# Performance work log

Hardware: AMD Instinct MI355X
Metric: run time of the kernel (lower is better)

The kernel has to match this reference:

```python
import jax, jax.numpy as jnp
import numpy as np

ENERGY_PERCENT = 0.8


def setup_inputs() -> dict:
    key = jax.random.key(0)
    B, T, C = 32, 4096, 128
    x = jax.random.normal(key, (B, T, C), dtype=jnp.float32)
    return {"x": x}


def reference(x):
    # x: [B, T, C]; FFT along time axis.
    T = x.shape[1]
    xf = jnp.fft.rfft(x, axis=1)                      # [B, F, C] complex
    energies = jnp.abs(xf) ** 2                       # [B, F, C]

    # Sort energies descending along freq axis (per batch, per channel).
    sorted_indices = jnp.argsort(-energies, axis=1)   # [B, F, C] int
    sorted_energies = jnp.take_along_axis(energies, sorted_indices, axis=1)

    total_energy = jnp.sum(energies, axis=1, keepdims=True)        # [B, 1, C]
    cumulative = jnp.cumsum(sorted_energies, axis=1)               # [B, F, C]

    # Smallest k such that cumulative energy exceeds energy_percent of total.
    exceeded = cumulative > total_energy * ENERGY_PERCENT          # [B, F, C] bool
    k = jnp.argmax(exceeded, axis=1) + 1                           # [B, C]

    # rank[b, f, c] = position of frequency f in the descending energy order;
    # this is the inverse permutation of sorted_indices (argsort of a permutation).
    rank = jnp.argsort(sorted_indices, axis=1)                     # [B, F, C]

    is_low_freq = rank < k[:, None, :]                             # [B, F, C]

    # Zero out the high-energy ("low-frequency") components -> residual x_var.
    mask = jnp.where(is_low_freq, 0.0, 1.0).astype(x.dtype)        # [B, F, C]
    x_var = jnp.fft.irfft(xf * mask, n=T, axis=1)                  # [B, T, C]
    x_inv = x - x_var
    return (x_var, x_inv)
```

## Files before the change

kernel.cpp:

```cpp
#include <hip/hip_runtime.h>


#define TLEN 4096
#define N2   2048
#define CCH  128
#define BB   32
#define NSER (BB * CCH)
#define HALF 16777216
#define PI_F 3.14159265358979323846f
#define NT   64
#define TS   64
#define SLAB (CCH * TS)

#define LP(i) ((i) + ((i) >> 5))

__device__ __forceinline__ void cmul(float& r, float& i, float br, float bi) {
  float tr = r * br - i * bi;
  i = r * bi + i * br;
  r = tr;
}

__device__ __forceinline__ void dft4(float vr[4], float vi[4], float s) {
  float t0r = vr[0] + vr[2], t0i = vi[0] + vi[2];
  float t1r = vr[0] - vr[2], t1i = vi[0] - vi[2];
  float t2r = vr[1] + vr[3], t2i = vi[1] + vi[3];
  float d3r = vr[1] - vr[3], d3i = vi[1] - vi[3];
  float t3r = -s * d3i, t3i = s * d3r;
  vr[0] = t0r + t2r; vi[0] = t0i + t2i;
  vr[1] = t1r + t3r; vi[1] = t1i + t3i;
  vr[2] = t0r - t2r; vi[2] = t0i - t2i;
  vr[3] = t1r - t3r; vi[3] = t1i - t3i;
}

__device__ __forceinline__ void dft8(float vr[8], float vi[8], float s) {
  float er[4]  = {vr[0], vr[2], vr[4], vr[6]};
  float ei[4]  = {vi[0], vi[2], vi[4], vi[6]};
  float odr[4] = {vr[1], vr[3], vr[5], vr[7]};
  float odi[4] = {vi[1], vi[3], vi[5], vi[7]};
  dft4(er, ei, s);
  dft4(odr, odi, s);
  const float c = 0.70710678118654752440f;
  float wr[4] = {1.0f, c, 0.0f, -c};
  float wi[4] = {0.0f, s * c, s, s * c};
  #pragma unroll
  for (int k = 0; k < 4; ++k) {
    float tr = wr[k] * odr[k] - wi[k] * odi[k];
    float ti = wr[k] * odi[k] + wi[k] * odr[k];
    vr[k]     = er[k] + tr; vi[k]     = ei[k] + ti;
    vr[k + 4] = er[k] - tr; vi[k + 4] = ei[k] - ti;
  }
}

__device__ __forceinline__ void stage8_first(float* zr, float* zi, int tid, float s) {
  float vr[8], vi[8];
  #pragma unroll
  for (int r = 0; r < 8; ++r) {
    int idx = LP(tid + (r << 8));
    vr[r] = zr[idx]; vi[r] = zi[idx];
  }
  dft8(vr, vi, s);
  __syncthreads();
  #pragma unroll
  for (int r = 0; r < 8; ++r) {
    int idx = LP((tid << 3) + r);
    zr[idx] = vr[r]; zi[idx] = vi[r];
  }
  __syncthreads();
}

template <int NS>
__device__ __forceinline__ void stage8_tw(float* zr, float* zi, int tid, float s) {
  int j = tid;
  int p = j & (NS - 1);
  float vr[8], vi[8];
  #pragma unroll
  for (int r = 0; r < 8; ++r) {
    int idx = LP(j + (r << 8));
    vr[r] = zr[idx]; vi[r] = zi[idx];
  }
  float ang = s * 6.28318530717958647692f * (float)p / (float)(NS * 8);
  float s1, c1; __sincosf(ang, &s1, &c1);
  float c2 = c1 * c1 - s1 * s1, s2 = 2.0f * c1 * s1;
  float c3 = c2 * c1 - s2 * s1, s3 = c2 * s1 + s2 * c1;
  float c4 = c2 * c2 - s2 * s2, s4 = 2.0f * c2 * s2;
  float c5 = c4 * c1 - s4 * s1, s5 = c4 * s1 + s4 * c1;
  float c6 = c4 * c2 - s4 * s2, s6 = c4 * s2 + s4 * c2;
  float c7 = c4 * c3 - s4 * s3, s7 = c4 * s3 + s4 * c3;
  cmul(vr[1], vi[1], c1, s1);
  cmul(vr[2], vi[2], c2, s2);
  cmul(vr[3], vi[3], c3, s3);
  cmul(vr[4], vi[4], c4, s4);
  cmul(vr[5], vi[5], c5, s5);
  cmul(vr[6], vi[6], c6, s6);
  cmul(vr[7], vi[7], c7, s7);
  dft8(vr, vi, s);
  __syncthreads();
  int idxD = ((j - p) << 3) + p;
  #pragma unroll
  for (int r = 0; r < 8; ++r) {
    int idx = LP(idxD + r * NS);
    zr[idx] = vr[r]; zi[idx] = vi[r];
  }
  __syncthreads();
}

__device__ __forceinline__ void stage4_last(float* zr, float* zi, int tid, float s) {
  #pragma unroll
  for (int half = 0; half < 2; ++half) {
    int j = tid + (half << 8);
    float ang = s * PI_F * (float)j * (1.0f / 1024.0f);
    float s1, c1; __sincosf(ang, &s1, &c1);
    float c2 = c1 * c1 - s1 * s1, s2 = 2.0f * c1 * s1;
    float c3 = c2 * c1 - s2 * s1, s3 = c2 * s1 + s2 * c1;
    float vr[4], vi[4];
    #pragma unroll
    for (int r = 0; r < 4; ++r) {
      int idx = LP(j + (r << 9));
      vr[r] = zr[idx]; vi[r] = zi[idx];
    }
    cmul(vr[1], vi[1], c1, s1);
    cmul(vr[2], vi[2], c2, s2);
    cmul(vr[3], vi[3], c3, s3);
    dft4(vr, vi, s);
    #pragma unroll
    for (int r = 0; r < 4; ++r) {
      int idx = LP(j + (r << 9));
      zr[idx] = vr[r]; zi[idx] = vi[r];
    }
  }
  __syncthreads();
}

__device__ __forceinline__ void fft2048(float* zr, float* zi, int tid, float s) {
  stage8_first(zr, zi, tid, s);
  stage8_tw<8>(zr, zi, tid, s);
  stage8_tw<64>(zr, zi, tid, s);
  stage4_last(zr, zi, tid, s);
}

__device__ __forceinline__ float block_sum(float v, float* red, int tid, int bank) {
  #pragma unroll
  for (int o = 32; o > 0; o >>= 1) v += __shfl_down(v, o, 64);
  if ((tid & 63) == 0) red[(bank << 2) + (tid >> 6)] = v;
  __syncthreads();
  int b4 = bank << 2;
  return red[b4] + red[b4 + 1] + red[b4 + 2] + red[b4 + 3];
}

__global__ __launch_bounds__(256, 8) void fourier_filter_series(const float* __restrict__ x,
                                                                float* __restrict__ buf) {
  __shared__ float zr[2113], zi[2113];
  __shared__ float red[8];
  int tid = threadIdx.x;

  int bid = blockIdx.x;
  int r = bid & 7;
  int m = bid >> 3;
  int b = m >> 4;
  int u = m & 15;
  int c = (((r + b) & 7) << 4) | u;

  const float* xp = x + ((size_t)b * TLEN) * CCH + c;
  #pragma unroll
  for (int jb = 0; jb < 2; ++jb) {
    float re[4], im[4];
    #pragma unroll
    for (int j = 0; j < 4; ++j) {
      int k = tid + (((jb << 2) + j) << 8);
      int off = k << 8;
      re[j] = xp[off];
      im[j] = xp[off + CCH];
    }
    #pragma unroll
    for (int j = 0; j < 4; ++j) {
      int k = tid + (((jb << 2) + j) << 8);
      zr[LP(k)] = re[j];
      zi[LP(k)] = im[j];
    }
  }
  __syncthreads();

  fft2048(zr, zi, tid, -1.0f);

  float eb[9];
  eb[8] = 0.0f;
  const float RC  = 0.92387953251128675613f;
  const float RSn = -0.38268343236508977173f;
  float ws, wc;
  __sincosf(-PI_F * (float)tid * (1.0f / 2048.0f), &ws, &wc);
  #pragma unroll
  for (int jj = 0; jj < 4; ++jj) {
    int k = tid + (jj << 8);
    int mkz = (N2 - k) & (N2 - 1);
    int ik = LP(k), im = LP(N2 - k);
    float akr = zr[ik],      aki = zi[ik];
    float bkr = zr[LP(mkz)], bki = zi[LP(mkz)];
    float Er  = 0.5f * (akr + bkr);
    float Ei  = 0.5f * (aki - bki);
    float Or_ = 0.5f * (aki + bki);
    float Oi  = 0.5f * (bkr - akr);
    float tr = wc * Or_ - ws * Oi;
    float ti = wc * Oi + ws * Or_;
    float x0r = Er + tr, x0i = Ei + ti;
    float x1r = Er - tr, x1i = ti - Ei;
    zr[ik] = x0r; zi[ik] = x0i;
    zr[im] = x1r; zi[im] = x1i;
    eb[2 * jj]     = x0r * x0r + x0i * x0i;
    eb[2 * jj + 1] = x1r * x1r + x1i * x1i;
    float nwc = wc * RC - ws * RSn;
    ws = wc * RSn + ws * RC; wc = nwc;
  }
  if (tid == 0) {
    int i4 = LP(1024);
    float re = zr[i4], im_ = zi[i4];
    zi[i4] = -im_;
    eb[8] = re * re + im_ * im_;
  }

  float tloc = 0.0f;
  #pragma unroll
  for (int s = 0; s < 9; ++s) tloc += eb[s];
  float total = block_sum(tloc, red, tid, 0);
  float thresh = 0.8f * total;

  unsigned lo = 0u, hi = 0x7F7FFFFFu;
  for (int it = 0; it < 31; ++it) {
    unsigned mid = (lo + hi + 1u) >> 1;
    float tau = __uint_as_float(mid);
    float loc = 0.0f;
    #pragma unroll
    for (int s = 0; s < 9; ++s) loc += (eb[s] >= tau) ? eb[s] : 0.0f;
    float ssum = block_sum(loc, red, tid, (it + 1) & 1);
    if (ssum > thresh) lo = mid; else hi = mid - 1;
  }
  float tau = __uint_as_float(lo);

  const float RSp = 0.38268343236508977173f;
  __sincosf(PI_F * (float)tid * (1.0f / 2048.0f), &ws, &wc);
  #pragma unroll
  for (int jj = 0; jj < 4; ++jj) {
    int k = tid + (jj << 8);
    int ik = LP(k), im = LP(N2 - k);
    float xkr = zr[ik], xki = zi[ik];
    float xmr = zr[im], xmi = zi[im];
    float ekk = xkr * xkr + xki * xki;
    float emm = xmr * xmr + xmi * xmi;
    if (ekk >= tau) { xkr = 0.0f; xki = 0.0f; }
    if (emm >= tau) { xmr = 0.0f; xmi = 0.0f; }
    float Er = 0.5f * (xkr + xmr);
    float Ei = 0.5f * (xki - xmi);
    float Br = 0.5f * (xkr - xmr);
    float Bi = 0.5f * (xki + xmi);
    float Or_ = wc * Br - ws * Bi;
    float Oi  = wc * Bi + ws * Br;
    zr[ik] = Er - Oi;  zi[ik] = Ei + Or_;
    zr[im] = Er + Oi;  zi[im] = Or_ - Ei;
    float nwc = wc * RC - ws * RSp;
    ws = wc * RSp + ws * RC; wc = nwc;
  }
  if (tid == 0) {
    int i4 = LP(1024);
    float re = zr[i4], im_ = zi[i4];
    float e = re * re + im_ * im_;
    if (e >= tau) { re = 0.0f; im_ = 0.0f; }
    zr[i4] = re; zi[i4] = -im_;
  }
  __syncthreads();

  fft2048(zr, zi, tid, 1.0f);

  float* bufp = buf + (size_t)b * (NT * SLAB) + (size_t)c * TS;
  const float scale = 1.0f / 2048.0f;
  #pragma unroll
  for (int j = 0; j < 8; ++j) {
    int k = tid + (j << 8);
    int off = ((k >> 5) << 13) + ((k & 31) << 1);
    float2 v;
    v.x = zr[LP(k)] * scale;
    v.y = zi[LP(k)] * scale;
    *(float2*)(bufp + off) = v;
  }
}

__global__ __launch_bounds__(512) void finalize_t(const float* __restrict__ buf, const float* __restrict__ x,
                                                  float* __restrict__ xvar, float* __restrict__ xinv) {
  __shared__ float lds[TS * 132];
  int tb = blockIdx.x, b = blockIdx.y;
  const float* ip = buf + ((size_t)b * NT + tb) * SLAB;
  #pragma unroll
  for (int it = 0; it < 4; ++it) {
    int idx = threadIdx.x + (it << 9);
    int c = idx >> 4, s4 = (idx & 15) << 2;
    float4 v = *(const float4*)(ip + c * TS + s4);
    int cs = c ^ (s4 & 28);
    lds[(s4 + 0) * 132 + cs] = v.x;
    lds[(s4 + 1) * 132 + cs] = v.y;
    lds[(s4 + 2) * 132 + cs] = v.z;
    lds[(s4 + 3) * 132 + cs] = v.w;
  }
  __syncthreads();
  size_t rowbase = ((size_t)b * TLEN + (size_t)tb * TS) * CCH;
  #pragma unroll
  for (int it = 0; it < 4; ++it) {
    int idx = threadIdx.x + (it << 9);
    int t = idx >> 5, c4 = (idx & 31) << 2;
    int key = ((t >> 2) & 7) << 2;
    float4 v = *(const float4*)(&lds[t * 132 + (c4 ^ key)]);
    size_t off = rowbase + (size_t)t * CCH + c4;
    float4 xv = *(const float4*)(x + off);
    *(float4*)(xvar + off) = v;
    *(float4*)(xinv + off) = make_float4(xv.x - v.x, xv.y - v.y, xv.z - v.z, xv.w - v.w);
  }
}

extern "C" void kernel_launch(void* const* d_in, const int* in_sizes, int n_in,
                              void* d_out, int out_size, void* d_ws, size_t ws_size,
                              hipStream_t stream) {
  const float* x = (const float*)d_in[0];
  float* out  = (float*)d_out;
  float* xvar = out;
  float* xinv = out + HALF;

  bool use_ws = ws_size >= (size_t)HALF * sizeof(float);
  float* buf = use_ws ? (float*)d_ws : xinv;

  fourier_filter_series<<<NSER, 256, 0, stream>>>(x, buf);
  dim3 tgrid(NT, BB);
  finalize_t<<<tgrid, 512, 0, stream>>>(buf, x, xvar, xinv);
}
```

Before: 305.2 us.

## Fuse FFT filter and finalize into one kernel processing four channels per block

Merges the per-series FFT filter kernel and the transpose/finalize kernel into one kernel. Each 1024-thread block handles four adjacent channels, one 256-thread group per channel. Input is loaded with float4 reads across the four channels, and x_var and x_inv are written directly from shared memory, which removes the intermediate workspace buffer and its extra global round trip. In exchange the block is much larger. The group reductions now take block-wide __syncthreads, so the four groups stall on each other through the 31-step threshold search, and the float4 accesses are only 16 bytes per time row.

```diff
diff --git a/kernel.cpp b/kernel.cpp
--- a/kernel.cpp
+++ b/kernel.cpp
@@ -5,14 +5,11 @@
 #define N2   2048
 #define CCH  128
 #define BB   32
-#define NSER (BB * CCH)
 #define HALF 16777216
 #define PI_F 3.14159265358979323846f
-#define NT   64
-#define TS   64
-#define SLAB (CCH * TS)
 
 #define LP(i) ((i) + ((i) >> 5))
+#define ZLEN 2113
 
 __device__ __forceinline__ void cmul(float& r, float& i, float br, float bi) {
   float tr = r * br - i * bi;
@@ -138,63 +135,67 @@
   stage4_last(zr, zi, tid, s);
 }
 
-__device__ __forceinline__ float block_sum(float v, float* red, int tid, int bank) {
+__device__ __forceinline__ float group_sum(float v, float* redg, int tg, int bank) {
   #pragma unroll
   for (int o = 32; o > 0; o >>= 1) v += __shfl_down(v, o, 64);
-  if ((tid & 63) == 0) red[(bank << 2) + (tid >> 6)] = v;
+  if ((tg & 63) == 0) redg[(bank << 2) + (tg >> 6)] = v;
   __syncthreads();
   int b4 = bank << 2;
-  return red[b4] + red[b4 + 1] + red[b4 + 2] + red[b4 + 3];
-}
-
-__global__ __launch_bounds__(256, 8) void fourier_filter_series(const float* __restrict__ x,
-                                                                float* __restrict__ buf) {
-  __shared__ float zr[2113], zi[2113];
-  __shared__ float red[8];
-  int tid = threadIdx.x;
+  return redg[b4] + redg[b4 + 1] + redg[b4 + 2] + redg[b4 + 3];
+}
+
+__global__ __launch_bounds__(1024, 8) void fourier_filter_fused(const float* __restrict__ x,
+                                                                float* __restrict__ xvar,
+                                                                float* __restrict__ xinv) {
+  __shared__ float z[2][4][ZLEN];
+  __shared__ float red[64];
+
+  int tidx = threadIdx.x;
 
   int bid = blockIdx.x;
   int r = bid & 7;
   int m = bid >> 3;
-  int b = m >> 4;
-  int u = m & 15;
-  int c = (((r + b) & 7) << 4) | u;
-
-  const float* xp = x + ((size_t)b * TLEN) * CCH + c;
-  #pragma unroll
-  for (int jb = 0; jb < 2; ++jb) {
-    float re[4], im[4];
-    #pragma unroll
-    for (int j = 0; j < 4; ++j) {
-      int k = tid + (((jb << 2) + j) << 8);
-      int off = k << 8;
-      re[j] = xp[off];
-      im[j] = xp[off + CCH];
-    }
-    #pragma unroll
-    for (int j = 0; j < 4; ++j) {
-      int k = tid + (((jb << 2) + j) << 8);
-      zr[LP(k)] = re[j];
-      zi[LP(k)] = im[j];
-    }
-  }
-  __syncthreads();
-
-  fft2048(zr, zi, tid, -1.0f);
+  int b = m >> 2;
+  int ql = m & 3;
+  int cg = (((r + b) & 7) << 2) | ql;
+  int cbase = cg << 2;
+
+  const float* xp = x + (size_t)b * (TLEN * CCH) + cbase;
+
+  #pragma unroll
+  for (int it = 0; it < 4; ++it) {
+    int t = tidx + (it << 10);
+    float4 v = *(const float4*)(xp + (size_t)t * CCH);
+    float* dst = &z[t & 1][0][0];
+    int k = LP(t >> 1);
+    dst[k]            = v.x;
+    dst[ZLEN + k]     = v.y;
+    dst[2 * ZLEN + k] = v.z;
+    dst[3 * ZLEN + k] = v.w;
+  }
+  __syncthreads();
+
+  int g  = tidx >> 8;
+  int tg = tidx & 255;
+  float* Zr = z[0][g];
+  float* Zi = z[1][g];
+  float* redg = red + (g << 3);
+
+  fft2048(Zr, Zi, tg, -1.0f);
 
   float eb[9];
   eb[8] = 0.0f;
   const float RC  = 0.92387953251128675613f;
   const float RSn = -0.38268343236508977173f;
   float ws, wc;
-  __sincosf(-PI_F * (float)tid * (1.0f / 2048.0f), &ws, &wc);
+  __sincosf(-PI_F * (float)tg * (1.0f / 2048.0f), &ws, &wc);
   #pragma unroll
   for (int jj = 0; jj < 4; ++jj) {
-    int k = tid + (jj << 8);
+    int k = tg + (jj << 8);
     int mkz = (N2 - k) & (N2 - 1);
     int ik = LP(k), im = LP(N2 - k);
-    float akr = zr[ik],      aki = zi[ik];
-    float bkr = zr[LP(mkz)], bki = zi[LP(mkz)];
+    float akr = Zr[ik],      aki = Zi[ik];
+    float bkr = Zr[LP(mkz)], bki = Zi[LP(mkz)];
     float Er  = 0.5f * (akr + bkr);
     float Ei  = 0.5f * (aki - bki);
     float Or_ = 0.5f * (aki + bki);
@@ -203,24 +204,24 @@
     float ti = wc * Oi + ws * Or_;
     float x0r = Er + tr, x0i = Ei + ti;
     float x1r = Er - tr, x1i = ti - Ei;
-    zr[ik] = x0r; zi[ik] = x0i;
-    zr[im] = x1r; zi[im] = x1i;
+    Zr[ik] = x0r; Zi[ik] = x0i;
+    Zr[im] = x1r; Zi[im] = x1i;
     eb[2 * jj]     = x0r * x0r + x0i * x0i;
     eb[2 * jj + 1] = x1r * x1r + x1i * x1i;
     float nwc = wc * RC - ws * RSn;
     ws = wc * RSn + ws * RC; wc = nwc;
   }
-  if (tid == 0) {
+  if (tg == 0) {
     int i4 = LP(1024);
-    float re = zr[i4], im_ = zi[i4];
-    zi[i4] = -im_;
+    float re = Zr[i4], im_ = Zi[i4];
+    Zi[i4] = -im_;
     eb[8] = re * re + im_ * im_;
   }
 
   float tloc = 0.0f;
   #pragma unroll
   for (int s = 0; s < 9; ++s) tloc += eb[s];
-  float total = block_sum(tloc, red, tid, 0);
+  float total = group_sum(tloc, redg, tg, 0);
   float thresh = 0.8f * total;
 
   unsigned lo = 0u, hi = 0x7F7FFFFFu;
@@ -230,19 +231,19 @@
     float loc = 0.0f;
     #pragma unroll
     for (int s = 0; s < 9; ++s) loc += (eb[s] >= tau) ? eb[s] : 0.0f;
-    float ssum = block_sum(loc, red, tid, (it + 1) & 1);
+    float ssum = group_sum(loc, redg, tg, (it + 1) & 1);
     if (ssum > thresh) lo = mid; else hi = mid - 1;
   }
   float tau = __uint_as_float(lo);
 
   const float RSp = 0.38268343236508977173f;
-  __sincosf(PI_F * (float)tid * (1.0f / 2048.0f), &ws, &wc);
+  __sincosf(PI_F * (float)tg * (1.0f / 2048.0f), &ws, &wc);
   #pragma unroll
   for (int jj = 0; jj < 4; ++jj) {
-    int k = tid + (jj << 8);
+    int k = tg + (jj << 8);
     int ik = LP(k), im = LP(N2 - k);
-    float xkr = zr[ik], xki = zi[ik];
-    float xmr = zr[im], xmi = zi[im];
+    float xkr = Zr[ik], xki = Zi[ik];
+    float xmr = Zr[im], xmi = Zi[im];
     float ekk = xkr * xkr + xki * xki;
     float emm = xmr * xmr + xmi * xmi;
     if (ekk >= tau) { xkr = 0.0f; xki = 0.0f; }
@@ -253,60 +254,35 @@
     float Bi = 0.5f * (xki + xmi);
     float Or_ = wc * Br - ws * Bi;
     float Oi  = wc * Bi + ws * Br;
-    zr[ik] = Er - Oi;  zi[ik] = Ei + Or_;
-    zr[im] = Er + Oi;  zi[im] = Or_ - Ei;
+    Zr[ik] = Er - Oi;  Zi[ik] = Ei + Or_;
+    Zr[im] = Er + Oi;  Zi[im] = Or_ - Ei;
     float nwc = wc * RC - ws * RSp;
     ws = wc * RSp + ws * RC; wc = nwc;
   }
-  if (tid == 0) {
+  if (tg == 0) {
     int i4 = LP(1024);
-    float re = zr[i4], im_ = zi[i4];
+    float re = Zr[i4], im_ = Zi[i4];
     float e = re * re + im_ * im_;
     if (e >= tau) { re = 0.0f; im_ = 0.0f; }
-    zr[i4] = re; zi[i4] = -im_;
-  }
-  __syncthreads();
-
-  fft2048(zr, zi, tid, 1.0f);
-
-  float* bufp = buf + (size_t)b * (NT * SLAB) + (size_t)c * TS;
+    Zr[i4] = re; Zi[i4] = -im_;
+  }
+  __syncthreads();
+
+  fft2048(Zr, Zi, tg, 1.0f);
+
   const float scale = 1.0f / 2048.0f;
-  #pragma unroll
-  for (int j = 0; j < 8; ++j) {
-    int k = tid + (j << 8);
-    int off = ((k >> 5) << 13) + ((k & 31) << 1);
-    float2 v;
-    v.x = zr[LP(k)] * scale;
-    v.y = zi[LP(k)] * scale;
-    *(float2*)(bufp + off) = v;
-  }
-}
-
-__global__ __launch_bounds__(512) void finalize_t(const float* __restrict__ buf, const float* __restrict__ x,
-                                                  float* __restrict__ xvar, float* __restrict__ xinv) {
-  __shared__ float lds[TS * 132];
-  int tb = blockIdx.x, b = blockIdx.y;
-  const float* ip = buf + ((size_t)b * NT + tb) * SLAB;
+  size_t base = (size_t)b * (TLEN * CCH) + cbase;
   #pragma unroll
   for (int it = 0; it < 4; ++it) {
-    int idx = threadIdx.x + (it << 9);
-    int c = idx >> 4, s4 = (idx & 15) << 2;
-    float4 v = *(const float4*)(ip + c * TS + s4);
-    int cs = c ^ (s4 & 28);
-    lds[(s4 + 0) * 132 + cs] = v.x;
-    lds[(s4 + 1) * 132 + cs] = v.y;
-    lds[(s4 + 2) * 132 + cs] = v.z;
-    lds[(s4 + 3) * 132 + cs] = v.w;
-  }
-  __syncthreads();
-  size_t rowbase = ((size_t)b * TLEN + (size_t)tb * TS) * CCH;
-  #pragma unroll
-  for (int it = 0; it < 4; ++it) {
-    int idx = threadIdx.x + (it << 9);
-    int t = idx >> 5, c4 = (idx & 31) << 2;
-    int key = ((t >> 2) & 7) << 2;
-    float4 v = *(const float4*)(&lds[t * 132 + (c4 ^ key)]);
-    size_t off = rowbase + (size_t)t * CCH + c4;
+    int t = tidx + (it << 10);
+    const float* src = &z[t & 1][0][0];
+    int k = LP(t >> 1);
+    float4 v;
+    v.x = src[k]            * scale;
+    v.y = src[ZLEN + k]     * scale;
+    v.z = src[2 * ZLEN + k] * scale;
+    v.w = src[3 * ZLEN + k] * scale;
+    size_t off = base + (size_t)t * CCH;
     float4 xv = *(const float4*)(x + off);
     *(float4*)(xvar + off) = v;
     *(float4*)(xinv + off) = make_float4(xv.x - v.x, xv.y - v.y, xv.z - v.z, xv.w - v.w);
@@ -321,10 +297,6 @@
   float* xvar = out;
   float* xinv = out + HALF;
 
-  bool use_ws = ws_size >= (size_t)HALF * sizeof(float);
-  float* buf = use_ws ? (float*)d_ws : xinv;
-
-  fourier_filter_series<<<NSER, 256, 0, stream>>>(x, buf);
-  dim3 tgrid(NT, BB);
-  finalize_t<<<tgrid, 512, 0, stream>>>(buf, x, xvar, xinv);
-}
+  (void)d_ws; (void)ws_size;
+  fourier_filter_fused<<<BB * 32, 1024, 0, stream>>>(x, xvar, xinv);
+}
```

Measured after the change: 290.6 us. -4.8%, faster.
